# Kernel tuning notes

Measured on AMD Instinct MI355X. Metric: run time of the kernel, lower is better.

Reference implementation:

```python
import jax, jax.numpy as jnp
import numpy as np

DIM_V, DIM_T, DIM_OUT, NUM_HEADS = 1024, 1024, 1024, 16
HEAD_DIM = DIM_OUT // NUM_HEADS
BETA = 1.0  # module multiplies scores by self.beta (=1); self.scale is unused


def setup_inputs() -> dict:
    key = jax.random.key(0)
    ks = jax.random.split(key, 12)
    B, N1, N2 = 8, 256, 4096
    E = jax.random.normal(ks[0], (B, N1, DIM_T), dtype=jnp.float32)
    I = jax.random.normal(ks[1], (B, N2, DIM_V), dtype=jnp.float32)
    s = 0.02
    # Conv1d(kernel_size=1) == linear; weights stored [out, in], bias [out]
    q_w = jax.random.normal(ks[2], (DIM_OUT, DIM_T), dtype=jnp.float32) * s
    q_b = jnp.zeros((DIM_OUT,), dtype=jnp.float32)
    k_w = jax.random.normal(ks[3], (DIM_OUT, DIM_V), dtype=jnp.float32) * s
    k_b = jnp.zeros((DIM_OUT,), dtype=jnp.float32)
    v_w = jax.random.normal(ks[4], (DIM_OUT, DIM_V), dtype=jnp.float32) * s
    v_b = jnp.zeros((DIM_OUT,), dtype=jnp.float32)
    p_w = jax.random.normal(ks[5], (DIM_OUT, DIM_OUT), dtype=jnp.float32) * s
    p_b = jnp.zeros((DIM_OUT,), dtype=jnp.float32)
    return {"E": E, "I": I, "q_w": q_w, "q_b": q_b, "k_w": k_w, "k_b": k_b,
            "v_w": v_w, "v_b": v_b, "p_w": p_w, "p_b": p_b}


def reference(E, I, q_w, q_b, k_w, k_b, v_w, v_b, p_w, p_b):
    B, N1, _ = E.shape
    _, N2, _ = I.shape
    # 1x1 conv projections == dense layers over channel dim
    Q = (jnp.einsum('bnc,oc->bno', E, q_w) + q_b).reshape(B, N1, NUM_HEADS, HEAD_DIM)
    K = (jnp.einsum('bmc,oc->bmo', I, k_w) + k_b).reshape(B, N2, NUM_HEADS, HEAD_DIM)
    V = (jnp.einsum('bmc,oc->bmo', I, v_w) + v_b).reshape(B, N2, NUM_HEADS, HEAD_DIM)
    # cross-attention scores [B, H, N1, N2]
    attn = jnp.einsum('bnhd,bmhd->bhnm', Q, K) * BETA
    attn = jax.nn.softmax(attn, axis=-1)
    U = jnp.einsum('bhnm,bmhd->bnhd', attn, V).reshape(B, N1, DIM_OUT)
    U = jnp.einsum('bnc,oc->bno', U, p_w) + p_b
    U = U / jnp.linalg.norm(U, axis=-1, keepdims=True)
    return jnp.concatenate([E, U], axis=2)  # [B, N1, dim_t + dim_out]
```

## Files before the change

### kernel.cpp

```cpp
#include <hip/hip_runtime.h>
#include <hip/hip_bf16.h>
#include <stdint.h>


typedef __bf16 bf16_t;
typedef __attribute__((ext_vector_type(8))) __bf16 bf16x8;
typedef __attribute__((ext_vector_type(4))) float f32x4;

#define DEVINL __device__ __forceinline__

DEVINL f32x4 mfma16(bf16x8 a, bf16x8 b, f32x4 c) {
  return __builtin_amdgcn_mfma_f32_16x16x32_bf16(a, b, c, 0, 0, 0);
}

DEVINL bf16x8 load8(const bf16_t* p) { return *(const bf16x8*)p; }
DEVINL bf16x8 load8(const float* p) {
  const float4 u = *(const float4*)p;
  const float4 v = *(const float4*)(p + 4);
  bf16x8 r;
  r[0] = (bf16_t)u.x; r[1] = (bf16_t)u.y; r[2] = (bf16_t)u.z; r[3] = (bf16_t)u.w;
  r[4] = (bf16_t)v.x; r[5] = (bf16_t)v.y; r[6] = (bf16_t)v.z; r[7] = (bf16_t)v.w;
  return r;
}

DEVINL uint32_t pack_bf16(float a, float b) {
  union { bf16_t h[2]; uint32_t u; } x;
  x.h[0] = (bf16_t)a; x.h[1] = (bf16_t)b;
  return x.u;
}

DEVINL void async16(const void* g, void* l) {
  typedef const __attribute__((address_space(1))) unsigned int* gp1;
  typedef __attribute__((address_space(3))) unsigned int* lp3;
  __builtin_amdgcn_global_load_lds((gp1)(uintptr_t)g,
                                   (lp3)(uint32_t)(uintptr_t)l, 16, 0, 0);
}

__global__ __launch_bounds__(256) void cvt_f32_bf16(
    const float* __restrict__ src, bf16_t* __restrict__ dst, int n8) {
  const int i = blockIdx.x * 256 + threadIdx.x;
  if (i < n8) *(bf16x8*)(dst + (size_t)i * 8) = load8(src + (size_t)i * 8);
}

template <int MODE>
__global__ __launch_bounds__(256) void gemm_bt_async(
    const bf16_t* __restrict__ A, const bf16_t* __restrict__ B,
    const float* __restrict__ bias, bf16_t* __restrict__ C,
    int M, int N, int K) {
  __shared__ bf16_t As[128 * 32];
  __shared__ bf16_t Bs[128 * 32];
  const int tid = threadIdx.x;
  const int w = tid >> 6, lane = tid & 63, quad = lane >> 4, l16 = lane & 15;
  const int bm = blockIdx.x * 128, bn = blockIdx.y * 128;
  const int wm = (w & 1) * 64, wn = (w >> 1) * 64;
  const int srow = tid >> 2;
  const int swz = ((tid & 3) ^ (srow & 3)) * 8;

  const bf16_t* Ag0 = A + (size_t)(bm + srow) * K + swz;
  const bf16_t* Ag1 = Ag0 + (size_t)64 * K;
  const bf16_t* Bg0 = B + (size_t)(bn + srow) * K + swz;
  const bf16_t* Bg1 = Bg0 + (size_t)64 * K;
  bf16_t* Al0 = As + tid * 8;
  bf16_t* Al1 = As + 64 * 32 + tid * 8;
  bf16_t* Bl0 = Bs + tid * 8;
  bf16_t* Bl1 = Bs + 64 * 32 + tid * 8;

  f32x4 acc[4][4] = {};

  for (int k0 = 0; k0 < K; k0 += 32) {
    async16(Ag0 + k0, Al0);
    async16(Ag1 + k0, Al1);
    async16(Bg0 + k0, Bl0);
    async16(Bg1 + k0, Bl1);
    __syncthreads();
    bf16x8 af[4], bfr[4];
#pragma unroll
    for (int mt = 0; mt < 4; mt++) {
      const int r = wm + mt * 16 + l16;
      af[mt] = *(const bf16x8*)(As + r * 32 + ((quad ^ (r & 3)) * 8));
    }
#pragma unroll
    for (int nt = 0; nt < 4; nt++) {
      const int r = wn + nt * 16 + l16;
      bfr[nt] = *(const bf16x8*)(Bs + r * 32 + ((quad ^ (r & 3)) * 8));
    }
#pragma unroll
    for (int mt = 0; mt < 4; mt++)
#pragma unroll
      for (int nt = 0; nt < 4; nt++)
        acc[mt][nt] = mfma16(af[mt], bfr[nt], acc[mt][nt]);
    __syncthreads();
  }

#pragma unroll
  for (int mt = 0; mt < 4; mt++) {
#pragma unroll
    for (int nt = 0; nt < 4; nt++) {
      const int gm0 = bm + wm + mt * 16 + quad * 4;
      const int gn = bn + wn + nt * 16 + l16;
#pragma unroll
      for (int r = 0; r < 4; r++) {
        const int gm = gm0 + r;
        C[(size_t)gm * N + gn] =
            (bf16_t)(acc[mt][nt][r] + bias[MODE == 1 ? gm : gn]);
      }
    }
  }
}

template <int MODE, typename TA, typename TB>
__global__ __launch_bounds__(256) void gemm_bt_reg(
    const TA* __restrict__ A, const TB* __restrict__ B,
    const float* __restrict__ bias, void* __restrict__ Cv,
    int M, int N, int K) {
  __shared__ bf16_t As[128 * 32];
  __shared__ bf16_t Bs[128 * 32];
  const int tid = threadIdx.x;
  const int w = tid >> 6, lane = tid & 63, quad = lane >> 4, l16 = lane & 15;
  const int bm = blockIdx.x * 128, bn = blockIdx.y * 128;
  const int wm = (w & 1) * 64, wn = (w >> 1) * 64;
  const int srow = tid >> 2;
  const int swz = ((tid & 3) ^ (srow & 3)) * 8;

  const TA* Ag0 = A + (size_t)(bm + srow) * K + swz;
  const TA* Ag1 = Ag0 + (size_t)64 * K;
  const TB* Bg0 = B + (size_t)(bn + srow) * K + swz;
  const TB* Bg1 = Bg0 + (size_t)64 * K;
  bf16_t* Al0 = As + tid * 8;
  bf16_t* Al1 = As + 64 * 32 + tid * 8;
  bf16_t* Bl0 = Bs + tid * 8;
  bf16_t* Bl1 = Bs + 64 * 32 + tid * 8;

  f32x4 acc[4][4] = {};

  for (int k0 = 0; k0 < K; k0 += 32) {
    const bf16x8 a0 = load8(Ag0 + k0);
    const bf16x8 a1 = load8(Ag1 + k0);
    const bf16x8 b0 = load8(Bg0 + k0);
    const bf16x8 b1 = load8(Bg1 + k0);
    *(bf16x8*)Al0 = a0;
    *(bf16x8*)Al1 = a1;
    *(bf16x8*)Bl0 = b0;
    *(bf16x8*)Bl1 = b1;
    __syncthreads();
    bf16x8 af[4], bfr[4];
#pragma unroll
    for (int mt = 0; mt < 4; mt++) {
      const int r = wm + mt * 16 + l16;
      af[mt] = *(const bf16x8*)(As + r * 32 + ((quad ^ (r & 3)) * 8));
    }
#pragma unroll
    for (int nt = 0; nt < 4; nt++) {
      const int r = wn + nt * 16 + l16;
      bfr[nt] = *(const bf16x8*)(Bs + r * 32 + ((quad ^ (r & 3)) * 8));
    }
#pragma unroll
    for (int mt = 0; mt < 4; mt++)
#pragma unroll
      for (int nt = 0; nt < 4; nt++)
        acc[mt][nt] = mfma16(af[mt], bfr[nt], acc[mt][nt]);
    __syncthreads();
  }

#pragma unroll
  for (int mt = 0; mt < 4; mt++) {
#pragma unroll
    for (int nt = 0; nt < 4; nt++) {
      const int gm0 = bm + wm + mt * 16 + quad * 4;
      const int gn = bn + wn + nt * 16 + l16;
#pragma unroll
      for (int r = 0; r < 4; r++) {
        const int gm = gm0 + r;
        float v = acc[mt][nt][r] + bias[MODE == 1 ? gm : gn];
        if (MODE == 2)
          ((float*)Cv)[(size_t)gm * N + gn] = v;
        else
          ((bf16_t*)Cv)[(size_t)gm * N + gn] = (bf16_t)v;
      }
    }
  }
}

__global__ __launch_bounds__(256) void attn_split(
    const bf16_t* __restrict__ QU, const bf16_t* __restrict__ Kbuf,
    const bf16_t* __restrict__ Vtbuf, float* __restrict__ opart,
    float* __restrict__ mls) {
  __shared__ bf16_t Ks[64 * 64];
  __shared__ bf16_t Vs[64 * 64];
  __shared__ bf16_t Ps[4][16 * 64];
  const int tid = threadIdx.x;
  const int w = tid >> 6, lane = tid & 63, quad = lane >> 4, l16 = lane & 15;
  const int flat = blockIdx.x;
  const int qt = flat >> 9, s = (flat >> 7) & 3, h = (flat >> 3) & 15, b = flat & 7;

  const int qlocal = qt * 64 + w * 16 + l16;
  const bf16_t* qbase = QU + (size_t)(b * 256 + qlocal) * 1024 + h * 64 + quad * 8;
  const bf16x8 qf0 = *(const bf16x8*)(qbase);
  const bf16x8 qf1 = *(const bf16x8*)(qbase + 32);

  const int srow = tid >> 3;
  const int swz = ((tid & 7) ^ (srow & 7)) * 8;
  const bf16_t* Kg =
      Kbuf + (size_t)(b * 4096 + s * 1024 + srow) * 1024 + h * 64 + swz;
  const bf16_t* Vg =
      Vtbuf + (size_t)(h * 64 + srow) * 32768 + b * 4096 + s * 1024 + swz;

  f32x4 o[4] = {};
  float m = -1e30f, l = 0.f;
  const float L2E = 1.4426950408889634f;

  bf16x8 kv0 = *(const bf16x8*)(Kg);
  bf16x8 kv1 = *(const bf16x8*)(Kg + (size_t)32 * 1024);
  bf16x8 vv0 = *(const bf16x8*)(Vg);
  bf16x8 vv1 = *(const bf16x8*)(Vg + (size_t)32 * 32768);

  for (int kt = 0; kt < 16; kt++) {
    __syncthreads();
    *(bf16x8*)(Ks + tid * 8) = kv0;
    *(bf16x8*)(Ks + 32 * 64 + tid * 8) = kv1;
    *(bf16x8*)(Vs + tid * 8) = vv0;
    *(bf16x8*)(Vs + 32 * 64 + tid * 8) = vv1;
    __syncthreads();
    if (kt < 15) {
      const size_t ko = (size_t)(kt + 1) * 64;
      kv0 = *(const bf16x8*)(Kg + ko * 1024);
      kv1 = *(const bf16x8*)(Kg + (ko + 32) * 1024);
      vv0 = *(const bf16x8*)(Vg + ko);
      vv1 = *(const bf16x8*)(Vg + ko + (size_t)32 * 32768);
    }

    f32x4 st[4];
#pragma unroll
    for (int nt = 0; nt < 4; nt++) {
      const int key = nt * 16 + l16;
      const bf16x8 kf0 = *(const bf16x8*)(Ks + key * 64 + ((quad ^ (key & 7)) * 8));
      const bf16x8 kf1 = *(const bf16x8*)(Ks + key * 64 + (((quad + 4) ^ (key & 7)) * 8));
      f32x4 z = {0.f, 0.f, 0.f, 0.f};
      z = mfma16(kf0, qf0, z);
      st[nt] = mfma16(kf1, qf1, z);
    }

    float mx = st[0][0];
#pragma unroll
    for (int nt = 0; nt < 4; nt++)
#pragma unroll
      for (int r = 0; r < 4; r++) mx = fmaxf(mx, st[nt][r]);
    mx = fmaxf(mx, __shfl_xor(mx, 16));
    mx = fmaxf(mx, __shfl_xor(mx, 32));
    const float mnew = fmaxf(m, mx);
    const float alpha = exp2f((m - mnew) * L2E);

    float rs = 0.f;
#pragma unroll
    for (int nt = 0; nt < 4; nt++) {
      const float p0 = exp2f((st[nt][0] - mnew) * L2E);
      const float p1 = exp2f((st[nt][1] - mnew) * L2E);
      const float p2 = exp2f((st[nt][2] - mnew) * L2E);
      const float p3 = exp2f((st[nt][3] - mnew) * L2E);
      rs += (p0 + p1) + (p2 + p3);
      uint2 pkv;
      pkv.x = pack_bf16(p0, p1);
      pkv.y = pack_bf16(p2, p3);
      *(uint2*)(&Ps[w][l16 * 64 + (((nt * 4 + quad) ^ l16) * 4)]) = pkv;
    }
    rs += __shfl_xor(rs, 16);
    rs += __shfl_xor(rs, 32);
    l = l * alpha + rs;
    m = mnew;
#pragma unroll
    for (int dt = 0; dt < 4; dt++) {
      o[dt][0] *= alpha; o[dt][1] *= alpha;
      o[dt][2] *= alpha; o[dt][3] *= alpha;
    }

#pragma unroll
    for (int ck = 0; ck < 2; ck++) {
      const int c0 = ck * 8 + quad * 2;
      union { uint2 ab[2]; bf16x8 v; } pf;
      pf.ab[0] = *(const uint2*)(&Ps[w][l16 * 64 + ((c0 ^ l16) * 4)]);
      pf.ab[1] = *(const uint2*)(&Ps[w][l16 * 64 + (((c0 + 1) ^ l16) * 4)]);
#pragma unroll
      for (int dt = 0; dt < 4; dt++) {
        const int row = dt * 16 + l16;
        const bf16x8 vf = *(const bf16x8*)(
            Vs + row * 64 + (((ck * 4 + quad) ^ (row & 7)) * 8));
        o[dt] = mfma16(vf, pf.v, o[dt]);
      }
    }
  }

  const int pr = ((b * 16 + h) << 8) | qlocal;
  if (quad == 0) {
    mls[((size_t)s * 32768 + pr) * 2 + 0] = m;
    mls[((size_t)s * 32768 + pr) * 2 + 1] = l;
  }
#pragma unroll
  for (int dt = 0; dt < 4; dt++)
    *(f32x4*)(opart + ((size_t)s * 32768 + pr) * 64 + dt * 16 + quad * 4) = o[dt];
}

__global__ __launch_bounds__(256) void attn_combine(
    const float* __restrict__ opart, const float* __restrict__ mls,
    bf16_t* __restrict__ QU) {
  const int w = threadIdx.x >> 6, lane = threadIdx.x & 63;
  const int pr = blockIdx.x * 4 + w;
  const float L2E = 1.4426950408889634f;
  float ms[4], ls[4];
#pragma unroll
  for (int s = 0; s < 4; s++) {
    ms[s] = mls[((size_t)s * 32768 + pr) * 2 + 0];
    ls[s] = mls[((size_t)s * 32768 + pr) * 2 + 1];
  }
  const float M = fmaxf(fmaxf(ms[0], ms[1]), fmaxf(ms[2], ms[3]));
  float L = 0.f, acc = 0.f;
#pragma unroll
  for (int s = 0; s < 4; s++) {
    const float e = exp2f((ms[s] - M) * L2E);
    L += ls[s] * e;
    acc += e * opart[((size_t)s * 32768 + pr) * 64 + lane];
  }
  const int b = pr >> 12, h = (pr >> 8) & 15, q = pr & 255;
  QU[(size_t)(b * 256 + q) * 1024 + h * 64 + lane] =
      (bf16_t)(acc / fmaxf(L, 1e-30f));
}

__global__ __launch_bounds__(256) void attn_old(
    bf16_t* QU, const bf16_t* __restrict__ Kbuf,
    const bf16_t* __restrict__ Vtbuf, int hg, int G, int Kst) {
  __shared__ bf16_t Ks[64 * 64];
  __shared__ bf16_t Vs[64 * 64];
  __shared__ bf16_t Ps[4][16 * 64];
  const int tid = threadIdx.x;
  const int w = tid >> 6, lane = tid & 63, quad = lane >> 4, l16 = lane & 15;
  const int flat = blockIdx.x;
  const int qt = flat / (8 * G);
  const int rem = flat - qt * 8 * G;
  const int hh = rem % G, b = rem / G;
  const int h = hg + hh;

  const int qrow = b * 256 + qt * 64 + w * 16 + l16;
  const bf16_t* qbase = QU + (size_t)qrow * 1024 + h * 64 + quad * 8;
  const bf16x8 qf0 = *(const bf16x8*)(qbase);
  const bf16x8 qf1 = *(const bf16x8*)(qbase + 32);

  const int srow = tid >> 3;
  const int swz = ((tid & 7) ^ (srow & 7)) * 8;
  const bf16_t* Kg = Kbuf + (size_t)(b * 4096 + srow) * Kst + hh * 64 + swz;
  const bf16_t* Vg = Vtbuf + (size_t)(hh * 64 + srow) * 32768 + b * 4096 + swz;

  f32x4 o[4] = {};
  float mrow[4] = {-1e30f, -1e30f, -1e30f, -1e30f};
  float lrow[4] = {0.f, 0.f, 0.f, 0.f};
  const float L2E = 1.4426950408889634f;

  bf16x8 kv0 = *(const bf16x8*)(Kg);
  bf16x8 kv1 = *(const bf16x8*)(Kg + (size_t)32 * Kst);
  bf16x8 vv0 = *(const bf16x8*)(Vg);
  bf16x8 vv1 = *(const bf16x8*)(Vg + (size_t)32 * 32768);

  for (int kt = 0; kt < 64; kt++) {
    __syncthreads();
    *(bf16x8*)(Ks + tid * 8) = kv0;
    *(bf16x8*)(Ks + 32 * 64 + tid * 8) = kv1;
    *(bf16x8*)(Vs + tid * 8) = vv0;
    *(bf16x8*)(Vs + 32 * 64 + tid * 8) = vv1;
    __syncthreads();
    if (kt < 63) {
      const size_t ko = (size_t)(kt + 1) * 64;
      kv0 = *(const bf16x8*)(Kg + ko * Kst);
      kv1 = *(const bf16x8*)(Kg + (ko + 32) * Kst);
      vv0 = *(const bf16x8*)(Vg + ko);
      vv1 = *(const bf16x8*)(Vg + ko + (size_t)32 * 32768);
    }

    f32x4 s[4];
#pragma unroll
    for (int nt = 0; nt < 4; nt++) {
      const int key = nt * 16 + l16;
      const bf16x8 kf0 = *(const bf16x8*)(Ks + key * 64 + ((quad ^ (key & 7)) * 8));
      const bf16x8 kf1 = *(const bf16x8*)(Ks + key * 64 + (((quad + 4) ^ (key & 7)) * 8));
      f32x4 z = {0.f, 0.f, 0.f, 0.f};
      z = mfma16(qf0, kf0, z);
      s[nt] = mfma16(qf1, kf1, z);
    }

    float mnew[4], alpha[4], rsum[4];
#pragma unroll
    for (int r = 0; r < 4; r++) {
      float mx = fmaxf(fmaxf(s[0][r], s[1][r]), fmaxf(s[2][r], s[3][r]));
      mx = fmaxf(mx, __shfl_xor(mx, 1));
      mx = fmaxf(mx, __shfl_xor(mx, 2));
      mx = fmaxf(mx, __shfl_xor(mx, 4));
      mx = fmaxf(mx, __shfl_xor(mx, 8));
      mnew[r] = fmaxf(mrow[r], mx);
      alpha[r] = exp2f((mrow[r] - mnew[r]) * L2E);
      rsum[r] = 0.f;
    }
#pragma unroll
    for (int nt = 0; nt < 4; nt++) {
      const int key = nt * 16 + l16;
#pragma unroll
      for (int r = 0; r < 4; r++) {
        const float p = exp2f((s[nt][r] - mnew[r]) * L2E);
        rsum[r] += p;
        const int q = quad * 4 + r;
        Ps[w][q * 64 + (((key >> 3) ^ (q & 7)) * 8) + (key & 7)] = (bf16_t)p;
      }
    }
#pragma unroll
    for (int r = 0; r < 4; r++) {
      rsum[r] += __shfl_xor(rsum[r], 1);
      rsum[r] += __shfl_xor(rsum[r], 2);
      rsum[r] += __shfl_xor(rsum[r], 4);
      rsum[r] += __shfl_xor(rsum[r], 8);
      lrow[r] = lrow[r] * alpha[r] + rsum[r];
      mrow[r] = mnew[r];
    }
#pragma unroll
    for (int nt = 0; nt < 4; nt++) {
      o[nt][0] *= alpha[0]; o[nt][1] *= alpha[1];
      o[nt][2] *= alpha[2]; o[nt][3] *= alpha[3];
    }

    __syncthreads();

    const bf16x8 pf0 = *(const bf16x8*)(&Ps[w][l16 * 64 + ((quad ^ (l16 & 7)) * 8)]);
    const bf16x8 pf1 = *(const bf16x8*)(&Ps[w][l16 * 64 + (((quad + 4) ^ (l16 & 7)) * 8)]);
#pragma unroll
    for (int nt = 0; nt < 4; nt++) {
      const int d = nt * 16 + l16;
      const bf16x8 vf0 = *(const bf16x8*)(Vs + d * 64 + ((quad ^ (d & 7)) * 8));
      const bf16x8 vf1 = *(const bf16x8*)(Vs + d * 64 + (((quad + 4) ^ (d & 7)) * 8));
      o[nt] = mfma16(pf0, vf0, o[nt]);
      o[nt] = mfma16(pf1, vf1, o[nt]);
    }
  }

  float inv[4];
#pragma unroll
  for (int r = 0; r < 4; r++) inv[r] = 1.0f / fmaxf(lrow[r], 1e-30f);
#pragma unroll
  for (int nt = 0; nt < 4; nt++) {
#pragma unroll
    for (int r = 0; r < 4; r++) {
      const int row = b * 256 + qt * 64 + w * 16 + quad * 4 + r;
      QU[(size_t)row * 1024 + h * 64 + nt * 16 + l16] = (bf16_t)(o[nt][r] * inv[r]);
    }
  }
}

__global__ __launch_bounds__(256) void norm_concat(
    const float* __restrict__ E, const float* __restrict__ P,
    float* __restrict__ out) {
  const int row = blockIdx.x, tid = threadIdx.x;
  const int w = tid >> 6, lane = tid & 63;

  *(float4*)(out + (size_t)row * 2048 + tid * 4) =
      *(const float4*)(E + (size_t)row * 1024 + tid * 4);

  const float4 p = *(const float4*)(P + (size_t)row * 1024 + tid * 4);
  float ss = p.x * p.x + p.y * p.y + p.z * p.z + p.w * p.w;
#pragma unroll
  for (int m = 1; m <= 32; m <<= 1) ss += __shfl_xor(ss, m);
  __shared__ float red[4];
  if (lane == 0) red[w] = ss;
  __syncthreads();
  const float rn = rsqrtf(fmaxf(red[0] + red[1] + red[2] + red[3], 1e-30f));
  float4 q;
  q.x = p.x * rn; q.y = p.y * rn; q.z = p.z * rn; q.w = p.w * rn;
  *(float4*)(out + (size_t)row * 2048 + 1024 + tid * 4) = q;
}

extern "C" void kernel_launch(void* const* d_in, const int* in_sizes, int n_in,
                              void* d_out, int out_size, void* d_ws, size_t ws_size,
                              hipStream_t stream) {
  (void)in_sizes; (void)n_in; (void)out_size;
  const float* E   = (const float*)d_in[0];
  const float* I   = (const float*)d_in[1];
  const float* q_w = (const float*)d_in[2];
  const float* q_b = (const float*)d_in[3];
  const float* k_w = (const float*)d_in[4];
  const float* k_b = (const float*)d_in[5];
  const float* v_w = (const float*)d_in[6];
  const float* v_b = (const float*)d_in[7];
  const float* p_w = (const float*)d_in[8];
  const float* p_b = (const float*)d_in[9];
  float* out = (float*)d_out;
  char* ws = (char*)d_ws;

  if (ws_size >= (200ull << 20)) {
    bf16_t* QU    = (bf16_t*)(ws);
    bf16_t* k_wbf = (bf16_t*)(ws + (4u << 20));
    bf16_t* v_wbf = (bf16_t*)(ws + (6u << 20));
    bf16_t* Ibf   = (bf16_t*)(ws + (8u << 20));
    float*  Pf    = (float*)(ws + (8u << 20));
    float*  opart = (float*)(ws + (16u << 20));
    float*  mls   = (float*)(ws + (52u << 20));
    bf16_t* Kbuf  = (bf16_t*)(ws + (72u << 20));
    bf16_t* Vtbuf = (bf16_t*)(ws + (136u << 20));

    cvt_f32_bf16<<<16384, 256, 0, stream>>>(I, Ibf, 32768 * 1024 / 8);
    cvt_f32_bf16<<<512, 256, 0, stream>>>(k_w, k_wbf, 1024 * 1024 / 8);
    cvt_f32_bf16<<<512, 256, 0, stream>>>(v_w, v_wbf, 1024 * 1024 / 8);

    gemm_bt_reg<0, float, float><<<dim3(16, 8), 256, 0, stream>>>(
        E, q_w, q_b, QU, 2048, 1024, 1024);
    gemm_bt_async<0><<<dim3(256, 8), 256, 0, stream>>>(
        Ibf, k_wbf, k_b, Kbuf, 32768, 1024, 1024);
    gemm_bt_async<1><<<dim3(8, 256), 256, 0, stream>>>(
        v_wbf, Ibf, v_b, Vtbuf, 1024, 32768, 1024);
    attn_split<<<2048, 256, 0, stream>>>(QU, Kbuf, Vtbuf, opart, mls);
    attn_combine<<<8192, 256, 0, stream>>>(opart, mls, QU);
    gemm_bt_reg<2, bf16_t, float><<<dim3(16, 8), 256, 0, stream>>>(
        QU, p_w, p_b, Pf, 2048, 1024, 1024);
    norm_concat<<<2048, 256, 0, stream>>>(E, Pf, out);
  } else {
    int G = 2;
    if (ws_size >= (133ull << 20)) G = 16;
    else if (ws_size >= (69ull << 20)) G = 8;
    else if (ws_size >= (37ull << 20)) G = 4;
    bf16_t* QU    = (bf16_t*)(ws);
    bf16_t* Kbuf  = (bf16_t*)(ws + (4u << 20));
    bf16_t* Vtbuf = (bf16_t*)(ws + (4u << 20) + ((size_t)G << 22));
    float*  Pf    = (float*)(ws + (4u << 20));

    gemm_bt_reg<0, float, float><<<dim3(16, 8), 256, 0, stream>>>(
        E, q_w, q_b, QU, 2048, 1024, 1024);
    for (int hg = 0; hg < 16; hg += G) {
      const int Nh = G * 64;
      gemm_bt_reg<0, float, float><<<dim3(256, Nh / 128), 256, 0, stream>>>(
          I, k_w + (size_t)hg * 64 * 1024, k_b + hg * 64, Kbuf, 32768, Nh, 1024);
      gemm_bt_reg<1, float, float><<<dim3(Nh / 128, 256), 256, 0, stream>>>(
          v_w + (size_t)hg * 64 * 1024, I, v_b + hg * 64, Vtbuf, Nh, 32768, 1024);
      attn_old<<<32 * G, 256, 0, stream>>>(QU, Kbuf, Vtbuf, hg, G, Nh);
    }
    gemm_bt_reg<2, bf16_t, float><<<dim3(16, 8), 256, 0, stream>>>(
        QU, p_w, p_b, Pf, 2048, 1024, 1024);
    norm_concat<<<2048, 256, 0, stream>>>(E, Pf, out);
  }
}
```

Before: 615.5 us.

## Deepen K step to 64 and swizzle block order in K/V projection GEMMs

The async-LDS GEMM now loads two 32-wide K slices per iteration into separate LDS buffers, so it issues twice the MFMA work per pair of barriers. The launch becomes a flat 1D grid, and a block-index swizzle groups the 8 blocks along the N=1024 dimension so they run adjacently and share the A (I) tile in L2. The intent is to cut barrier and latency overhead and to improve L2 reuse of the large I matrix. In exchange LDS use doubles to 32 KB per block, which may lower occupancy.

```diff
diff --git a/kernel.cpp b/kernel.cpp
--- a/kernel.cpp
+++ b/kernel.cpp
@@ -47,48 +47,55 @@
     const bf16_t* __restrict__ A, const bf16_t* __restrict__ B,
     const float* __restrict__ bias, bf16_t* __restrict__ C,
     int M, int N, int K) {
-  __shared__ bf16_t As[128 * 32];
-  __shared__ bf16_t Bs[128 * 32];
+  __shared__ bf16_t As[2][128 * 32];
+  __shared__ bf16_t Bs[2][128 * 32];
   const int tid = threadIdx.x;
   const int w = tid >> 6, lane = tid & 63, quad = lane >> 4, l16 = lane & 15;
-  const int bm = blockIdx.x * 128, bn = blockIdx.y * 128;
+  const int bid = blockIdx.x;
+  const int swz = (bid & 7) * (int)(gridDim.x >> 3) + (bid >> 3);
+  const int big = swz >> 3, small = swz & 7;
+  const int bm = 128 * (MODE == 1 ? small : big);
+  const int bn = 128 * (MODE == 1 ? big : small);
   const int wm = (w & 1) * 64, wn = (w >> 1) * 64;
   const int srow = tid >> 2;
-  const int swz = ((tid & 3) ^ (srow & 3)) * 8;
-
-  const bf16_t* Ag0 = A + (size_t)(bm + srow) * K + swz;
+  const int sw8 = ((tid & 3) ^ (srow & 3)) * 8;
+
+  const bf16_t* Ag0 = A + (size_t)(bm + srow) * K + sw8;
   const bf16_t* Ag1 = Ag0 + (size_t)64 * K;
-  const bf16_t* Bg0 = B + (size_t)(bn + srow) * K + swz;
+  const bf16_t* Bg0 = B + (size_t)(bn + srow) * K + sw8;
   const bf16_t* Bg1 = Bg0 + (size_t)64 * K;
-  bf16_t* Al0 = As + tid * 8;
-  bf16_t* Al1 = As + 64 * 32 + tid * 8;
-  bf16_t* Bl0 = Bs + tid * 8;
-  bf16_t* Bl1 = Bs + 64 * 32 + tid * 8;
 
   f32x4 acc[4][4] = {};
 
-  for (int k0 = 0; k0 < K; k0 += 32) {
-    async16(Ag0 + k0, Al0);
-    async16(Ag1 + k0, Al1);
-    async16(Bg0 + k0, Bl0);
-    async16(Bg1 + k0, Bl1);
-    __syncthreads();
-    bf16x8 af[4], bfr[4];
-#pragma unroll
-    for (int mt = 0; mt < 4; mt++) {
-      const int r = wm + mt * 16 + l16;
-      af[mt] = *(const bf16x8*)(As + r * 32 + ((quad ^ (r & 3)) * 8));
-    }
-#pragma unroll
-    for (int nt = 0; nt < 4; nt++) {
-      const int r = wn + nt * 16 + l16;
-      bfr[nt] = *(const bf16x8*)(Bs + r * 32 + ((quad ^ (r & 3)) * 8));
-    }
-#pragma unroll
-    for (int mt = 0; mt < 4; mt++)
-#pragma unroll
-      for (int nt = 0; nt < 4; nt++)
-        acc[mt][nt] = mfma16(af[mt], bfr[nt], acc[mt][nt]);
+  for (int k0 = 0; k0 < K; k0 += 64) {
+    async16(Ag0 + k0, As[0] + tid * 8);
+    async16(Ag1 + k0, As[0] + 64 * 32 + tid * 8);
+    async16(Bg0 + k0, Bs[0] + tid * 8);
+    async16(Bg1 + k0, Bs[0] + 64 * 32 + tid * 8);
+    async16(Ag0 + k0 + 32, As[1] + tid * 8);
+    async16(Ag1 + k0 + 32, As[1] + 64 * 32 + tid * 8);
+    async16(Bg0 + k0 + 32, Bs[1] + tid * 8);
+    async16(Bg1 + k0 + 32, Bs[1] + 64 * 32 + tid * 8);
+    __syncthreads();
+#pragma unroll
+    for (int h = 0; h < 2; h++) {
+      bf16x8 af[4], bfr[4];
+#pragma unroll
+      for (int mt = 0; mt < 4; mt++) {
+        const int r = wm + mt * 16 + l16;
+        af[mt] = *(const bf16x8*)(As[h] + r * 32 + ((quad ^ (r & 3)) * 8));
+      }
+#pragma unroll
+      for (int nt = 0; nt < 4; nt++) {
+        const int r = wn + nt * 16 + l16;
+        bfr[nt] = *(const bf16x8*)(Bs[h] + r * 32 + ((quad ^ (r & 3)) * 8));
+      }
+#pragma unroll
+      for (int mt = 0; mt < 4; mt++)
+#pragma unroll
+        for (int nt = 0; nt < 4; nt++)
+          acc[mt][nt] = mfma16(af[mt], bfr[nt], acc[mt][nt]);
+    }
     __syncthreads();
   }
 
@@ -505,9 +512,9 @@
 
     gemm_bt_reg<0, float, float><<<dim3(16, 8), 256, 0, stream>>>(
         E, q_w, q_b, QU, 2048, 1024, 1024);
-    gemm_bt_async<0><<<dim3(256, 8), 256, 0, stream>>>(
+    gemm_bt_async<0><<<2048, 256, 0, stream>>>(
         Ibf, k_wbf, k_b, Kbuf, 32768, 1024, 1024);
-    gemm_bt_async<1><<<dim3(8, 256), 256, 0, stream>>>(
+    gemm_bt_async<1><<<2048, 256, 0, stream>>>(
         v_wbf, Ibf, v_b, Vtbuf, 1024, 32768, 1024);
     attn_split<<<2048, 256, 0, stream>>>(QU, Kbuf, Vtbuf, opart, mls);
     attn_combine<<<8192, 256, 0, stream>>>(opart, mls, QU);
```

Result: faster. 580.5 us (-5.7%).
